# Performance work log

Hardware: AMD Instinct MI355X
Metric: run time of the kernel (lower is better)

## Reference

```python
import jax, jax.numpy as jnp
import numpy as np
import math

N_HEAD = 16
N_EMBD = 2048
HEAD_DIM = 128
N_LAYER = 24
EPS = 1e-5


def _get_alibi_slopes(n_heads):
    def pow2(n):
        start = 2 ** (-2 ** (-(math.log2(n) - 3)))
        return [start * start ** i for i in range(n)]
    if math.log2(n_heads).is_integer():
        return pow2(n_heads)
    c = 2 ** math.floor(math.log2(n_heads))
    s = pow2(c)
    extra = _get_alibi_slopes(2 * c)
    return s + extra[0::2][: n_heads - c]

ALIBI_SLOPES = jnp.asarray(np.array(_get_alibi_slopes(N_HEAD), dtype=np.float32))  # (H,)


def rmsnorm(x, w, eps=EPS):
    # fp32 RMSNorm over last dim with affine weight (use_fp32=True path)
    xf = x.astype(jnp.float32)
    out = xf * jax.lax.rsqrt(jnp.mean(xf * xf, axis=-1, keepdims=True) + eps)
    return (out * w.astype(jnp.float32)).astype(x.dtype)


def setup_inputs() -> dict:
    key = jax.random.key(0)
    ks = jax.random.split(key, 8)
    B, T, C, H, D = 2, 2048, N_EMBD, N_HEAD, HEAD_DIM
    sc = 1.0 / math.sqrt(C)
    proj_std = 0.5 / math.sqrt(C) / math.sqrt(N_LAYER)
    return {
        "x": jax.random.normal(ks[0], (B, T, C), jnp.float32),
        "Wq": jax.random.normal(ks[1], (C, H * D), jnp.float32) * sc,
        "Wk": jax.random.normal(ks[2], (C, H * D), jnp.float32) * sc,
        "Wv": jax.random.normal(ks[3], (C, H * D), jnp.float32) * sc,
        "Wproj": jax.random.normal(ks[4], (H * D, C), jnp.float32) * proj_std,
        "q_rms_w": jnp.ones((D,), jnp.float32),
        "k_rms_w": jnp.ones((D,), jnp.float32),
        "subln_w": jnp.ones((D,), jnp.float32),
    }


def reference(x, Wq, Wk, Wv, Wproj, q_rms_w, k_rms_w, subln_w):
    B, T, C = x.shape
    H, D = N_HEAD, HEAD_DIM
    q = (x @ Wq).reshape(B, T, H, D)
    k = (x @ Wk).reshape(B, T, H, D)
    v = (x @ Wv).reshape(B, T, H, D)
    # QK RMSNorm over head_dim
    q = rmsnorm(q, q_rms_w)
    k = rmsnorm(k, k_rms_w)
    # ALiBi bias: -slope * max(i-j, 0), plus causal mask
    idx = jnp.arange(T)
    dist = jnp.maximum(idx[:, None] - idx[None, :], 0).astype(jnp.float32)  # (T,T)
    bias = -dist[None, :, :] * ALIBI_SLOPES[:, None, None]  # (H,T,T)
    causal = idx[:, None] >= idx[None, :]  # (T,T)
    scale = 1.0 / math.sqrt(D)
    scores = jnp.einsum("bthd,bshd->bhts", q, k) * scale + bias[None]  # (B,H,T,T)
    scores = jnp.where(causal[None, None], scores, -jnp.inf)
    attn = jax.nn.softmax(scores, axis=-1)
    y = jnp.einsum("bhts,bshd->bhtd", attn, v)  # (B,H,T,D)
    y = rmsnorm(y, subln_w)  # post-attention groupnorm (subln)
    y = y.transpose(0, 2, 1, 3).reshape(B, T, H * D)
    return y @ Wproj
```

## Files before the change

kernel.cpp:

```cpp
#include <hip/hip_runtime.h>
#include <hip/hip_bf16.h>

#define Bc 2
#define Tc 2048
#define Cc 2048
#define Hc 16
#define Dc 128
#define BTc 4096
#define NQ 6144
#define EPSc 1e-5f
#define QSCALE 0.08838834764831845f

typedef __attribute__((ext_vector_type(8))) short bf16x8;
typedef __attribute__((ext_vector_type(4))) short bf16x4;
typedef __attribute__((ext_vector_type(4))) float f32x4;

__device__ __forceinline__ f32x4 mfma16(bf16x8 a, bf16x8 b, f32x4 c) {
  return __builtin_amdgcn_mfma_f32_16x16x32_bf16(a, b, c, 0, 0, 0);
}

__device__ __forceinline__ void gload16(const void* g, void* l) {
  __builtin_amdgcn_global_load_lds(
      (const __attribute__((address_space(1))) void*)g,
      (__attribute__((address_space(3))) void*)l, 16, 0, 0);
}

__global__ __launch_bounds__(256) void k_xconv(const float* __restrict__ x,
                                               __hip_bfloat16* __restrict__ xb) {
  size_t i = ((size_t)blockIdx.x * 256 + threadIdx.x) * 4;
  float4 v = *(const float4*)(x + i);
  union { __hip_bfloat16 h[4]; bf16x4 v4; } u;
  u.h[0] = __float2bfloat16(v.x); u.h[1] = __float2bfloat16(v.y);
  u.h[2] = __float2bfloat16(v.z); u.h[3] = __float2bfloat16(v.w);
  *(bf16x4*)(xb + i) = u.v4;
}

__global__ __launch_bounds__(256) void k_wconv(const float* __restrict__ Wq,
    const float* __restrict__ Wk, const float* __restrict__ Wv,
    const float* __restrict__ Wp, __hip_bfloat16* __restrict__ Wqkv_t,
    __hip_bfloat16* __restrict__ Wproj_t) {
  __shared__ float tile[64][65];
  int z = blockIdx.z;
  const float* src = (z == 0) ? Wq : (z == 1) ? Wk : (z == 2) ? Wv : Wp;
  __hip_bfloat16* dst = (z < 3) ? (Wqkv_t + (size_t)z * Cc * Cc) : Wproj_t;
  int k0 = blockIdx.x * 64, n0 = blockIdx.y * 64;
  int c = threadIdx.x & 63, rb = threadIdx.x >> 6;
  for (int i = 0; i < 16; i++) {
    int r = rb * 16 + i;
    tile[r][c] = src[(size_t)(k0 + r) * Cc + n0 + c];
  }
  __syncthreads();
  for (int i = 0; i < 16; i++) {
    int r = rb * 16 + i;
    dst[(size_t)(n0 + r) * Cc + k0 + c] = __float2bfloat16(tile[c][r]);
  }
}

__device__ __forceinline__ void rdA4(bf16x8 (&d)[4], const char* p) {
#pragma unroll
  for (int m = 0; m < 4; m++) d[m] = *(const bf16x8*)(p + m * 1024);
}
__device__ __forceinline__ void rdB4(bf16x8 (&d)[4], const char* p) {
#pragma unroll
  for (int n = 0; n < 4; n++) d[n] = *(const bf16x8*)(p + n * 1024);
}
__device__ __forceinline__ void mm44(f32x4 (&acc)[4][4], const bf16x8 (&A_)[4],
                                     const bf16x8 (&B_)[4]) {
  __builtin_amdgcn_s_setprio(1);
#pragma unroll
  for (int m = 0; m < 4; m++)
#pragma unroll
    for (int n = 0; n < 4; n++)
      acc[m][n] = mfma16(A_[m], B_[n], acc[m][n]);
  __builtin_amdgcn_s_setprio(0);
}

template <typename OutT>
__global__ __launch_bounds__(512, 2) void k_gemm8b(const __hip_bfloat16* __restrict__ A,
    const __hip_bfloat16* __restrict__ Bt, OutT* __restrict__ Co,
    int M, int N) {
  constexpr int K = 2048;
  __shared__ __align__(16) char lds[147456];
  const int nbx = M >> 7;
  const int nwg = nbx * (N >> 8);
  const int wg = blockIdx.x;
  const int swz = (wg & 7) * (nwg >> 3) + (wg >> 3);
  const int bx = swz % nbx, by = swz / nbx;
  const int tid = threadIdx.x, lane = tid & 63, wid = tid >> 6;
  const int wr = wid >> 2, wc = wid & 3;
  const int lr = lane & 15, lg = lane >> 4;
  const int roff = lr * 64 + (lg ^ ((lr >> 1) & 3)) * 16;
  const int srow = wid * 16 + (lane >> 2);
  const int scol = (((lane & 3) ^ ((srow >> 1) & 3)) << 3);
  const __hip_bfloat16* Ag = A + (size_t)(bx * 128 + srow) * K + scol;
  const __hip_bfloat16* Bg = Bt + (size_t)(by * 256 + srow) * K + scol;
  char* ldsw = lds + wid * 1024;
  const size_t rstepB = (size_t)128 * K;
  const char* Ab = lds + wr * 4096 + roff;
  const char* Bb = lds + 16384 + wc * 4096 + roff;

#define STG_A(bufo, t, kk) gload16(Ag + (t) * 64 + (kk) * 32, \
                                   ldsw + (bufo) + (kk) * 8192)
#define STG_B(bufo, t, kk) { const __hip_bfloat16* g_ = Bg + (t) * 64 + (kk) * 32; \
    gload16(g_, ldsw + (bufo) + 16384 + (kk) * 16384);                              \
    gload16(g_ + rstepB, ldsw + (bufo) + 16384 + (kk) * 16384 + 8192); }
#define BARRIER asm volatile("s_barrier" ::: "memory")
#define VW6 asm volatile("s_waitcnt vmcnt(6)" ::: "memory")
#define VW0 asm volatile("s_waitcnt vmcnt(0)" ::: "memory")

  f32x4 acc[4][4];
#pragma unroll
  for (int m = 0; m < 4; m++)
#pragma unroll
    for (int n = 0; n < 4; n++) acc[m][n] = f32x4{0.f, 0.f, 0.f, 0.f};
  bf16x8 rA[4], rB[4];

#define TILE(RB, SB, TS, DOSTG, ENDW)                                   \
  {                                                                     \
    rdA4(rA, Ab + (RB));                                                \
    rdB4(rB, Bb + (RB));                                                \
    if (DOSTG) { STG_A((SB), (TS), 0); STG_B((SB), (TS), 0); }          \
    BARRIER;                                                            \
    mm44(acc, rA, rB);                                                  \
    BARRIER;                                                            \
    rdA4(rA, Ab + (RB) + 8192);                                         \
    rdB4(rB, Bb + (RB) + 16384);                                        \
    if (DOSTG) { STG_A((SB), (TS), 1); STG_B((SB), (TS), 1); }          \
    BARRIER;                                                            \
    mm44(acc, rA, rB);                                                  \
    ENDW;                                                               \
    BARRIER;                                                            \
  }

  STG_A(0, 0, 0); STG_B(0, 0, 0); STG_A(0, 0, 1); STG_B(0, 0, 1);
  STG_A(49152, 1, 0); STG_B(49152, 1, 0); STG_A(49152, 1, 1); STG_B(49152, 1, 1);
  VW6;
  BARRIER;

  for (int i = 0; i < 10; ++i) {
    const int t = 3 * i;
    TILE(0,     98304, t + 2, 1, VW6);
    TILE(49152, 0,     t + 3, 1, VW6);
    TILE(98304, 49152, t + 4, 1, VW6);
  }
  TILE(0,     0, 0, 0, VW0);
  TILE(49152, 0, 0, 0, (void)0);
#undef TILE
#undef STG_A
#undef STG_B
#undef BARRIER
#undef VW6
#undef VW0

  const int row0 = bx * 128 + wr * 64 + lg * 4;
  const int col0 = by * 256 + wc * 64 + lr;
#pragma unroll
  for (int m = 0; m < 4; m++)
#pragma unroll
    for (int n = 0; n < 4; n++) {
      size_t base = (size_t)(row0 + m * 16) * N + col0 + n * 16;
#pragma unroll
      for (int r = 0; r < 4; r++) {
        float v = acc[m][n][r];
        if constexpr (sizeof(OutT) == 2)
          Co[base + (size_t)r * N] = __float2bfloat16(v);
        else
          Co[base + (size_t)r * N] = v;
      }
    }
}

__global__ __launch_bounds__(256) void k_qkrms(__hip_bfloat16* __restrict__ QKV,
    const float* __restrict__ qw, const float* __restrict__ kw) {
  int bt = blockIdx.x;
  int w = threadIdx.x >> 6, lane = threadIdx.x & 63;
  int hv = blockIdx.y * 4 + w;
  const float* wt; int col; float extra;
  if (hv < 16) { wt = qw; col = hv * Dc;             extra = QSCALE; }
  else         { wt = kw; col = Cc + (hv - 16) * Dc; extra = 1.0f;   }
  __hip_bfloat16* p = QKV + (size_t)bt * NQ + col + lane * 2;
  float x0 = __bfloat162float(p[0]);
  float x1 = __bfloat162float(p[1]);
  float ss = x0 * x0 + x1 * x1;
  for (int m = 1; m < 64; m <<= 1) ss += __shfl_xor(ss, m);
  float sc = rsqrtf(ss * (1.0f / Dc) + EPSc) * extra;
  p[0] = __float2bfloat16(x0 * sc * wt[lane * 2]);
  p[1] = __float2bfloat16(x1 * sc * wt[lane * 2 + 1]);
}

__global__ __launch_bounds__(256) void k_vtrans(const __hip_bfloat16* __restrict__ QKV,
                                                __hip_bfloat16* __restrict__ Vt) {
  __shared__ __hip_bfloat16 tile[64][65];
  int bh = blockIdx.z, t0 = blockIdx.x * 64, d0 = blockIdx.y * 64;
  int b = bh >> 4, h = bh & 15;
  int c = threadIdx.x & 63, rb = threadIdx.x >> 6;
  for (int i = 0; i < 16; i++) {
    int r = rb * 16 + i;
    tile[r][c] = QKV[(size_t)(b * Tc + t0 + r) * NQ + 2 * Cc + h * Dc + d0 + c];
  }
  __syncthreads();
  for (int i = 0; i < 16; i++) {
    int r = rb * 16 + i;
    Vt[((size_t)bh * Dc + d0 + r) * Tc + t0 + c] = tile[c][r];
  }
}

__global__ __launch_bounds__(256, 2) void k_attn(const __hip_bfloat16* __restrict__ QKV,
    const __hip_bfloat16* __restrict__ Vt, const float* __restrict__ subw,
    __hip_bfloat16* __restrict__ Y) {
  __shared__ __align__(16) __hip_bfloat16 Ks[2][64][128];
  __shared__ __align__(16) __hip_bfloat16 Vs[2][128][64];
  __shared__ __align__(16) __hip_bfloat16 Plds[4][16][72];
  const int bh = blockIdx.x, pp = blockIdx.y;
  const int b = bh >> 4, h = bh & 15;
  const int w = threadIdx.x >> 6, lane = threadIdx.x & 63;
  const int lr = lane & 15, lg = lane >> 4;
  const float slope = exp2f(-0.5f * (float)(h + 1));
  const __hip_bfloat16* Kbase = QKV + (size_t)b * Tc * NQ + Cc + h * Dc;
  const __hip_bfloat16* Vbase = Vt + (size_t)bh * Dc * Tc;
  const int krow = (lane >> 4);
  const int kcolb = ((lane & 15) << 4);
  const int vrow = (lane >> 3);
  const int vcolb = ((lane & 7) << 4);
  f32x4 zero = {0.f, 0.f, 0.f, 0.f};

#define STAGE(bb, t)                                                              \
    {                                                                             \
      const int s0_ = (t) * 64;                                                   \
      for (int j = 0; j < 4; j++) {                                               \
        int row = w * 16 + j * 4 + krow;                                          \
        int cb = kcolb ^ ((row & 7) << 4);                                        \
        gload16(Kbase + (size_t)(s0_ + row) * NQ + (cb >> 1),                     \
                &Ks[bb][w * 16 + j * 4][0]);                                      \
      }                                                                           \
      for (int j = 0; j < 4; j++) {                                               \
        int row = w * 32 + j * 8 + vrow;                                          \
        int cb = vcolb ^ ((row & 7) << 4);                                        \
        gload16(Vbase + (size_t)row * Tc + s0_ + (cb >> 1),                       \
                &Vs[bb][w * 32 + j * 8][0]);                                      \
      }                                                                           \
    }
#define SBAR asm volatile("s_barrier" ::: "memory")
#define AVW8 asm volatile("s_waitcnt vmcnt(8)" ::: "memory")
#define AVW0 asm volatile("s_waitcnt vmcnt(0)" ::: "memory")
#define ALG0 asm volatile("s_waitcnt lgkmcnt(0)" ::: "memory")

  int buf = 0;
  for (int ti = 0; ti < 2; ti++) {
    const int qt = (ti == 0) ? (31 - pp) : pp;
    const int q0 = qt * 64 + w * 16;
    const int nchunk = qt + 1;
    bf16x8 aq[4];
    {
      const __hip_bfloat16* qb = QKV + (size_t)(b * Tc + q0 + lr) * NQ + h * Dc + lg * 8;
      for (int c = 0; c < 4; c++) aq[c] = *(const bf16x8*)(qb + c * 32);
    }
    f32x4 acc[8];
    for (int d = 0; d < 8; d++) acc[d] = zero;
    float mrow[4] = {-1e30f, -1e30f, -1e30f, -1e30f};
    float lrow[4] = {0.f, 0.f, 0.f, 0.f};

    SBAR;
    STAGE(buf, 0);
    for (int t = 0; t < nchunk; t++) {
      if (t + 1 < nchunk) { STAGE(buf ^ 1, t + 1); AVW8; }
      else                { AVW0; }
      SBAR;
      const int s0 = t * 64;
      f32x4 s[4];
      for (int ss = 0; ss < 4; ss++) s[ss] = zero;
      __builtin_amdgcn_s_setprio(1);
      for (int c = 0; c < 4; c++)
        for (int ss = 0; ss < 4; ss++) {
          int kr = ss * 16 + lr;
          const bf16x8 kf = *(const bf16x8*)
              &Ks[buf][kr][((c * 64 + lg * 16) ^ ((kr & 7) << 4)) >> 1];
          s[ss] = mfma16(aq[c], kf, s[ss]);
        }
      __builtin_amdgcn_s_setprio(0);
      float ps[4][4], mt[4];
      for (int r = 0; r < 4; r++) mt[r] = -1e30f;
      for (int ss = 0; ss < 4; ss++) {
        int jj = s0 + ss * 16 + lr;
        for (int r = 0; r < 4; r++) {
          int i = q0 + lg * 4 + r;
          float pv = (jj <= i) ? s[ss][r] - slope * (float)(i - jj) : -1e30f;
          ps[ss][r] = pv;
          mt[r] = fmaxf(mt[r], pv);
        }
      }
      for (int m = 1; m < 16; m <<= 1)
        for (int r = 0; r < 4; r++) mt[r] = fmaxf(mt[r], __shfl_xor(mt[r], m));
      float corr[4], rs[4];
      for (int r = 0; r < 4; r++) {
        float mn = fmaxf(mrow[r], mt[r]);
        corr[r] = __expf(mrow[r] - mn);
        mrow[r] = mn;
        rs[r] = 0.f;
      }
      for (int ss = 0; ss < 4; ss++)
        for (int r = 0; r < 4; r++) {
          float e = __expf(ps[ss][r] - mrow[r]);
          ps[ss][r] = e;
          rs[r] += e;
        }
      for (int m = 1; m < 16; m <<= 1)
        for (int r = 0; r < 4; r++) rs[r] += __shfl_xor(rs[r], m);
      for (int r = 0; r < 4; r++) lrow[r] = lrow[r] * corr[r] + rs[r];
      for (int d = 0; d < 8; d++)
        for (int r = 0; r < 4; r++) acc[d][r] *= corr[r];
      for (int ss = 0; ss < 4; ss++)
        for (int r = 0; r < 4; r++)
          Plds[w][lg * 4 + r][ss * 16 + lr] = __float2bfloat16(ps[ss][r]);
      bf16x8 pa0 = *(const bf16x8*)&Plds[w][lr][lg * 8];
      bf16x8 pa1 = *(const bf16x8*)&Plds[w][lr][32 + lg * 8];
      __builtin_amdgcn_s_setprio(1);
      for (int d = 0; d < 8; d++) {
        int vr = d * 16 + lr;
        const bf16x8 b0 = *(const bf16x8*)
            &Vs[buf][vr][((lg * 16) ^ ((vr & 7) << 4)) >> 1];
        const bf16x8 b1 = *(const bf16x8*)
            &Vs[buf][vr][((64 + lg * 16) ^ ((vr & 7) << 4)) >> 1];
        acc[d] = mfma16(pa0, b0, acc[d]);
        acc[d] = mfma16(pa1, b1, acc[d]);
      }
      __builtin_amdgcn_s_setprio(0);
      ALG0; SBAR;
      buf ^= 1;
    }
    float ssum[4] = {0.f, 0.f, 0.f, 0.f};
    for (int r = 0; r < 4; r++) {
      float rl = 1.0f / lrow[r];
      for (int d = 0; d < 8; d++) {
        float o = acc[d][r] * rl;
        acc[d][r] = o;
        ssum[r] += o * o;
      }
    }
    for (int m = 1; m < 16; m <<= 1)
      for (int r = 0; r < 4; r++) ssum[r] += __shfl_xor(ssum[r], m);
    float ms[4];
    for (int r = 0; r < 4; r++) ms[r] = rsqrtf(ssum[r] * (1.0f / Dc) + EPSc);
    for (int d = 0; d < 8; d++) {
      float wv = subw[d * 16 + lr];
      for (int r = 0; r < 4; r++) {
        float y = acc[d][r] * ms[r] * wv;
        Y[(size_t)(b * Tc + q0 + lg * 4 + r) * Cc + h * Dc + d * 16 + lr] =
            __float2bfloat16(y);
      }
    }
  }
#undef STAGE
#undef SBAR
#undef AVW8
#undef AVW0
#undef ALG0
}

extern "C" void kernel_launch(void* const* d_in, const int* in_sizes, int n_in,
                              void* d_out, int out_size, void* d_ws, size_t ws_size,
                              hipStream_t stream) {
  const float* x  = (const float*)d_in[0];
  const float* Wq = (const float*)d_in[1];
  const float* Wk = (const float*)d_in[2];
  const float* Wv = (const float*)d_in[3];
  const float* Wp = (const float*)d_in[4];
  const float* qw = (const float*)d_in[5];
  const float* kw = (const float*)d_in[6];
  const float* sw = (const float*)d_in[7];
  float* out = (float*)d_out;

  char* ws = (char*)d_ws;
  __hip_bfloat16* Xb    = (__hip_bfloat16*)(ws + 0);
  __hip_bfloat16* Wqkv  = (__hip_bfloat16*)(ws + 16777216);
  __hip_bfloat16* Wproj = (__hip_bfloat16*)(ws + 41943040);
  __hip_bfloat16* QKV   = (__hip_bfloat16*)(ws + 50331648);
  __hip_bfloat16* Vt    = (__hip_bfloat16*)(ws + 100663296);
  __hip_bfloat16* Yb    = (__hip_bfloat16*)(ws + 117440512);

  k_xconv<<<dim3((BTc * Cc) / 1024), 256, 0, stream>>>(x, Xb);
  k_wconv<<<dim3(32, 32, 4), 256, 0, stream>>>(Wq, Wk, Wv, Wp, Wqkv, Wproj);
  k_gemm8b<__hip_bfloat16><<<dim3((BTc / 128) * (NQ / 256)), 512, 0, stream>>>(
      Xb, Wqkv, QKV, BTc, NQ);
  k_qkrms<<<dim3(BTc, 8), 256, 0, stream>>>(QKV, qw, kw);
  k_vtrans<<<dim3(Tc / 64, Dc / 64, Bc * Hc), 256, 0, stream>>>(QKV, Vt);
  k_attn<<<dim3(Bc * Hc, 16), 256, 0, stream>>>(QKV, Vt, sw, Yb);
  k_gemm8b<float><<<dim3((BTc / 128) * (Cc / 256)), 512, 0, stream>>>(
      Yb, Wproj, out, BTc, Cc);
}
```

Before: 294.6 us.

## Add 4-wave 128x256 GEMM with triple-buffered LDS for QKV projection

Adds a new GEMM kernel that uses 4 waves (256 threads), each computing a 64x128 subtile with a 4x8 MFMA accumulator block. It stages tiles into LDS through direct global-to-LDS loads with a three-stage ring buffer and one barrier per k-step. The QKV projection is switched to it, while the output projection keeps the old 8-wave kernel. The goal is more register-level reuse per wave and deeper prefetch, at the cost of higher register pressure and fewer waves to hide latency.

```diff
diff --git a/kernel.cpp b/kernel.cpp
--- a/kernel.cpp
+++ b/kernel.cpp
@@ -54,6 +54,112 @@
     int r = rb * 16 + i;
     dst[(size_t)(n0 + r) * Cc + k0 + c] = __float2bfloat16(tile[c][r]);
   }
+}
+
+__device__ __forceinline__ void mm48(f32x4 (&acc)[4][8], const bf16x8 (&A_)[4],
+                                     const bf16x8 (&B_)[8]) {
+  __builtin_amdgcn_s_setprio(1);
+#pragma unroll
+  for (int m = 0; m < 4; m++)
+#pragma unroll
+    for (int n = 0; n < 8; n++)
+      acc[m][n] = mfma16(A_[m], B_[n], acc[m][n]);
+  __builtin_amdgcn_s_setprio(0);
+}
+
+template <typename OutT>
+__global__ __launch_bounds__(256, 2) void k_gemm4(const __hip_bfloat16* __restrict__ A,
+    const __hip_bfloat16* __restrict__ Bt, OutT* __restrict__ Co,
+    int M, int N) {
+  constexpr int K = 2048;
+  __shared__ __align__(16) char lds[73728];
+  const int nbx = M >> 7;
+  const int nwg = nbx * (N >> 8);
+  const int wg = blockIdx.x;
+  const int swz = (wg & 7) * (nwg >> 3) + (wg >> 3);
+  const int bx = swz % nbx, by = swz / nbx;
+  const int tid = threadIdx.x, lane = tid & 63, wid = tid >> 6;
+  const int wr = wid >> 1, wc = wid & 1;
+  const int lr = lane & 15, lg = lane >> 4;
+  const int xs = lg ^ ((lr >> 1) & 3);
+  const int aoffR = (wr * 64 + lr) * 64 + xs * 16;
+  const int boffR = 8192 + (wc * 128 + lr) * 64 + xs * 16;
+  const int srow = lane >> 2;
+  const int scolE = (((lane & 3) ^ ((lane >> 3) & 3)) << 3);
+  const __hip_bfloat16* Ag = A + (size_t)(bx * 128 + wid * 32 + srow) * K + scolE;
+  const __hip_bfloat16* Bg = Bt + (size_t)(by * 256 + wid * 64 + srow) * K + scolE;
+  const size_t rK16 = (size_t)16 * K;
+  char* dA = lds + wid * 2048;
+  char* dB = lds + 8192 + wid * 4096;
+
+#define STG(BUF, TS) {                                                   \
+    gload16(Ag + (TS) * 32,        dA + (BUF) * 24576);                  \
+    gload16(Ag + rK16 + (TS) * 32, dA + (BUF) * 24576 + 1024);           \
+    gload16(Bg + (TS) * 32,            dB + (BUF) * 24576);              \
+    gload16(Bg + rK16 + (TS) * 32,     dB + (BUF) * 24576 + 1024);       \
+    gload16(Bg + 2 * rK16 + (TS) * 32, dB + (BUF) * 24576 + 2048);       \
+    gload16(Bg + 3 * rK16 + (TS) * 32, dB + (BUF) * 24576 + 3072);       \
+  }
+#define BARRIER asm volatile("s_barrier" ::: "memory")
+#define VW6 asm volatile("s_waitcnt vmcnt(6)" ::: "memory")
+#define VW0 asm volatile("s_waitcnt vmcnt(0)" ::: "memory")
+
+  f32x4 acc[4][8];
+#pragma unroll
+  for (int m = 0; m < 4; m++)
+#pragma unroll
+    for (int n = 0; n < 8; n++) acc[m][n] = f32x4{0.f, 0.f, 0.f, 0.f};
+  bf16x8 rA[4], rB[8];
+
+#define PH(RB, SB, TS, DOSTG, ENDW) {                                    \
+    _Pragma("unroll")                                                    \
+    for (int m = 0; m < 4; m++)                                          \
+      rA[m] = *(const bf16x8*)(lds + (RB) * 24576 + aoffR + m * 1024);   \
+    _Pragma("unroll")                                                    \
+    for (int n = 0; n < 8; n++)                                          \
+      rB[n] = *(const bf16x8*)(lds + (RB) * 24576 + boffR + n * 1024);   \
+    if (DOSTG) STG((SB), (TS));                                          \
+    mm48(acc, rA, rB);                                                   \
+    ENDW;                                                                \
+    BARRIER;                                                             \
+  }
+
+  STG(0, 0); STG(1, 1);
+  VW6;
+  BARRIER;
+
+  for (int i = 0; i < 20; ++i) {
+    const int t = 3 * i;
+    PH(0, 2, t + 2, 1, VW6);
+    PH(1, 0, t + 3, 1, VW6);
+    PH(2, 1, t + 4, 1, VW6);
+  }
+  PH(0, 2, 62, 1, VW6);
+  PH(1, 0, 63, 1, VW6);
+  PH(2, 0, 0, 0, VW0);
+  PH(0, 0, 0, 0, (void)0);
+#undef PH
+#undef STG
+#undef BARRIER
+#undef VW6
+#undef VW0
+
+  const int row0 = bx * 128 + wr * 64 + lg * 4;
+  const int col0 = by * 256 + wc * 128 + lr;
+#pragma unroll
+  for (int m = 0; m < 4; m++)
+#pragma unroll
+    for (int n = 0; n < 8; n++) {
+      size_t base = (size_t)(row0 + m * 16) * N + col0 + n * 16;
+#pragma unroll
+      for (int r = 0; r < 4; r++) {
+        float v = acc[m][n][r];
+        if constexpr (sizeof(OutT) == 2)
+          Co[base + (size_t)r * N] = __float2bfloat16(v);
+        else
+          Co[base + (size_t)r * N] = v;
+      }
+    }
 }
 
 __device__ __forceinline__ void rdA4(bf16x8 (&d)[4], const char* p) {
@@ -380,7 +486,7 @@
 
   k_xconv<<<dim3((BTc * Cc) / 1024), 256, 0, stream>>>(x, Xb);
   k_wconv<<<dim3(32, 32, 4), 256, 0, stream>>>(Wq, Wk, Wv, Wp, Wqkv, Wproj);
-  k_gemm8b<__hip_bfloat16><<<dim3((BTc / 128) * (NQ / 256)), 512, 0, stream>>>(
+  k_gemm4<__hip_bfloat16><<<dim3((BTc / 128) * (NQ / 256)), 256, 0, stream>>>(
       Xb, Wqkv, QKV, BTc, NQ);
   k_qkrms<<<dim3(BTc, 8), 256, 0, stream>>>(QKV, qw, kw);
   k_vtrans<<<dim3(Tc / 64, Dc / 64, Bc * Hc), 256, 0, stream>>>(QKV, Vt);
```

Measured after the change: 279.8 us. 1.05x faster.
